# Kernel tuning notes

Measured on AMD Instinct MI355X. Metric: run time of the kernel, lower is better.

The kernel has to match this reference:

```python
import jax, jax.numpy as jnp
import numpy as np
import math

D = 1024
H = 16
EPS = 1e-5

def _layernorm(x, gamma, beta):
    mu = jnp.mean(x, axis=-1, keepdims=True)
    var = jnp.var(x, axis=-1, keepdims=True)
    return (x - mu) * jax.lax.rsqrt(var + EPS) * gamma + beta

def setup_inputs() -> dict:
    key = jax.random.key(0)
    ks = jax.random.split(key, 6)
    B, T = 2, 2048
    x = jax.random.normal(ks[0], (B, T, D), dtype=jnp.float32)
    s = 1.0 / math.sqrt(D)
    Wq = jax.random.normal(ks[1], (D, D), dtype=jnp.float32) * s
    Wk = jax.random.normal(ks[2], (D, D), dtype=jnp.float32) * s
    Wv = jax.random.normal(ks[3], (D, D), dtype=jnp.float32) * s
    gamma = jnp.ones((D,), dtype=jnp.float32)
    beta = jnp.zeros((D,), dtype=jnp.float32)
    return {"x": x, "Wq": Wq, "Wk": Wk, "Wv": Wv, "gamma": gamma, "beta": beta}

def reference(x, Wq, Wk, Wv, gamma, beta):
    B, T, Dm = x.shape
    hd = Dm // H
    xn = _layernorm(x, gamma, beta)
    # torch Linear (no bias): y = x @ W.T
    q = (xn @ Wq.T).reshape(B, T, H, hd)
    k = (xn @ Wk.T).reshape(B, T, H, hd)
    v = (xn @ Wv.T).reshape(B, T, H, hd)
    scale = 1.0 / math.sqrt(hd)
    att = jnp.einsum('bnhd,bmhd->bnmh', q, k) * scale  # B,T,T,H
    w = jax.nn.softmax(att, axis=2)  # softmax over key dim m
    y = jnp.einsum('bnmh,bmhd->bnhd', w, v).reshape(B, T, Dm)
    return x + y
```

## Files before the change

kernel.cpp:

```cpp
#include <hip/hip_runtime.h>
#include <hip/hip_bf16.h>
#include <stdint.h>

#define D_MODEL 1024
#define T_SEQ   2048
#define NB      2
#define NH      16
#define HD      64
#define MTOK    4096

typedef __bf16  bf16x8 __attribute__((ext_vector_type(8)));
typedef float   f32x4  __attribute__((ext_vector_type(4)));
typedef float   f32x16 __attribute__((ext_vector_type(16)));

#define GPTR(p) ((const __attribute__((address_space(1))) void*)(p))
#define LPTR(p) ((__attribute__((address_space(3))) void*)(p))

static __device__ __forceinline__ ushort f2bf(float f) {
    union { float f; uint32_t u; } c{f};
    uint32_t u = c.u;
    return (ushort)((u + 0x7fff + ((u >> 16) & 1)) >> 16);
}

static __device__ __forceinline__ unsigned cvt_pk_bf16(float lo, float hi) {
    unsigned r;
    asm("v_cvt_pk_bf16_f32 %0, %1, %2" : "=v"(r) : "v"(lo), "v"(hi));
    return r;
}

#if defined(__has_builtin)
#if __has_builtin(__builtin_amdgcn_exp2f)
#define FEXP2(x) __builtin_amdgcn_exp2f(x)
#endif
#endif
#ifndef FEXP2
static __device__ __forceinline__ float fexp2_asm(float x) {
    float r;
    asm("v_exp_f32 %0, %1" : "=v"(r) : "v"(x));
    return r;
}
#define FEXP2(x) fexp2_asm(x)
#endif

__global__ __launch_bounds__(256) void prep_kernel(const float* __restrict__ x,
                                                   const float* __restrict__ gamma,
                                                   const float* __restrict__ beta,
                                                   ushort* __restrict__ xn,
                                                   const float* __restrict__ a0,
                                                   const float* __restrict__ a1,
                                                   const float* __restrict__ a2,
                                                   ushort* __restrict__ o0,
                                                   ushort* __restrict__ o1,
                                                   ushort* __restrict__ o2) {
    int blk = blockIdx.x;
    int tid = threadIdx.x;
    if (blk >= MTOK) {
        int z = (blk - MTOK) >> 10;
        int cb = (blk - MTOK) & 1023;
        const float* a = (z == 0) ? a0 : (z == 1) ? a1 : a2;
        ushort* o = (z == 0) ? o0 : (z == 1) ? o1 : o2;
        int i = cb * 256 + tid;
        float4 v = ((const float4*)a)[i];
        ushort4 r;
        r.x = f2bf(v.x); r.y = f2bf(v.y); r.z = f2bf(v.z); r.w = f2bf(v.w);
        ((ushort4*)o)[i] = r;
        return;
    }
    int row = blk;
    const float4* xr = (const float4*)(x + (size_t)row * D_MODEL);
    float4 v = xr[tid];
    float s  = v.x + v.y + v.z + v.w;
    float ss = v.x * v.x + v.y * v.y + v.z * v.z + v.w * v.w;
    #pragma unroll
    for (int m = 1; m < 64; m <<= 1) {
        s  += __shfl_xor(s, m);
        ss += __shfl_xor(ss, m);
    }
    __shared__ float red[8];
    int w = tid >> 6, lane = tid & 63;
    if (lane == 0) { red[w] = s; red[4 + w] = ss; }
    __syncthreads();
    s  = red[0] + red[1] + red[2] + red[3];
    ss = red[4] + red[5] + red[6] + red[7];
    float mu   = s * (1.0f / D_MODEL);
    float var  = ss * (1.0f / D_MODEL) - mu * mu;
    float rstd = rsqrtf(var + 1e-5f);
    float4 g = ((const float4*)gamma)[tid];
    float4 b = ((const float4*)beta)[tid];
    ushort4 o;
    o.x = f2bf((v.x - mu) * rstd * g.x + b.x);
    o.y = f2bf((v.y - mu) * rstd * g.y + b.y);
    o.z = f2bf((v.z - mu) * rstd * g.z + b.z);
    o.w = f2bf((v.w - mu) * rstd * g.w + b.w);
    ((ushort4*)(xn + (size_t)row * D_MODEL))[tid] = o;
}

__global__ __launch_bounds__(256) void gemm_qkv(const ushort* __restrict__ A,
                                                const ushort* __restrict__ w0,
                                                const ushort* __restrict__ w1,
                                                const ushort* __restrict__ w2,
                                                ushort* __restrict__ c0,
                                                ushort* __restrict__ c1,
                                                ushort* __restrict__ c2,
                                                int M, int N, int K) {
    const ushort* Bw = (blockIdx.z == 0) ? w0 : (blockIdx.z == 1) ? w1 : w2;
    ushort* C = (blockIdx.z == 0) ? c0 : (blockIdx.z == 1) ? c1 : c2;

    __shared__ __align__(16) ushort lA[2][128 * 64];
    __shared__ __align__(16) ushort lB[2][128 * 64];
    int tid = threadIdx.x;
    int w = tid >> 6, lane = tid & 63;
    int wr = w >> 1, wc = w & 1;
    int l15 = lane & 15, l4 = lane >> 4;
    int row0 = blockIdx.x * 128, col0 = blockIdx.y * 128;

    f32x4 zero = {0.f, 0.f, 0.f, 0.f};
    f32x4 acc[4][4];
    #pragma unroll
    for (int i = 0; i < 4; ++i)
        #pragma unroll
        for (int j = 0; j < 4; ++j) acc[i][j] = zero;

    int sr  = tid >> 3;
    int scc = (((tid & 7) ^ (sr & 7)) << 3);
    int rch[2];
    rch[0] = ((l4)     ^ (l15 & 7)) << 4;
    rch[1] = ((4 + l4) ^ (l15 & 7)) << 4;

    auto STAGE = [&](int buf, int kt) {
        int k0 = kt * 64;
        #pragma unroll
        for (int i = 0; i < 4; ++i) {
            int r = i * 32 + sr;
            const ushort* ga = A + (size_t)(row0 + r) * K + k0 + scc;
            __builtin_amdgcn_global_load_lds(GPTR(ga), LPTR((char*)lA[buf] + i * 4096 + tid * 16), 16, 0, 0);
            const ushort* gb = Bw + (size_t)(col0 + r) * K + k0 + scc;
            __builtin_amdgcn_global_load_lds(GPTR(gb), LPTR((char*)lB[buf] + i * 4096 + tid * 16), 16, 0, 0);
        }
    };

    STAGE(0, 0);
    __syncthreads();

    int buf = 0;
    const int NK = K / 64;
    for (int kt = 0; kt < NK; ++kt) {
        if (kt + 1 < NK) STAGE(buf ^ 1, kt + 1);
        const char* la  = (const char*)lA[buf];
        const char* lb_ = (const char*)lB[buf];
        __builtin_amdgcn_s_setprio(1);
        #pragma unroll
        for (int ks = 0; ks < 2; ++ks) {
            bf16x8 af[4], bfr[4];
            #pragma unroll
            for (int i = 0; i < 4; ++i) {
                int ra = wr * 64 + i * 16 + l15;
                int rb = wc * 64 + i * 16 + l15;
                af[i]  = *(const bf16x8*)(la  + ra * 128 + rch[ks]);
                bfr[i] = *(const bf16x8*)(lb_ + rb * 128 + rch[ks]);
            }
            #pragma unroll
            for (int i = 0; i < 4; ++i)
                #pragma unroll
                for (int j = 0; j < 4; ++j)
                    acc[i][j] = __builtin_amdgcn_mfma_f32_16x16x32_bf16(af[i], bfr[j], acc[i][j], 0, 0, 0);
        }
        __builtin_amdgcn_s_setprio(0);
        __syncthreads();
        buf ^= 1;
    }

    if (blockIdx.z == 2) {
        #pragma unroll
        for (int i = 0; i < 4; ++i) {
            int rbase = row0 + wr * 64 + i * 16 + l4 * 4;
            #pragma unroll
            for (int j = 0; j < 4; ++j) {
                int col = col0 + wc * 64 + j * 16 + l15;
                ushort4 o4;
                o4.x = f2bf(acc[i][j][0]);
                o4.y = f2bf(acc[i][j][1]);
                o4.z = f2bf(acc[i][j][2]);
                o4.w = f2bf(acc[i][j][3]);
                *(ushort4*)&C[(size_t)col * M + rbase] = o4;
            }
        }
    } else {
        float sc = (blockIdx.z == 0) ? 0.18033688011112042f : 1.0f;
        #pragma unroll
        for (int i = 0; i < 4; ++i) {
            int rbase = row0 + wr * 64 + i * 16 + l4 * 4;
            #pragma unroll
            for (int j = 0; j < 4; ++j) {
                int col = col0 + wc * 64 + j * 16 + l15;
                #pragma unroll
                for (int r = 0; r < 4; ++r)
                    C[(size_t)(rbase + r) * N + col] = f2bf(acc[i][j][r] * sc);
            }
        }
    }
}

__global__ __launch_bounds__(512, 2) void attn_kernel(const ushort* __restrict__ Q,
                                                      const ushort* __restrict__ Km,
                                                      const ushort* __restrict__ Vt,
                                                      const float* __restrict__ x,
                                                      float* __restrict__ out) {
    int bid = blockIdx.x;
    int sw  = (bid & 7) * 32 + (bid >> 3);
    int qt = sw & 7, h = (sw >> 3) & 15, b = sw >> 7;

    int tid = threadIdx.x, w = tid >> 6, lane = tid & 63;
    int l31 = lane & 31, hh = lane >> 5, x7 = lane & 7;
    size_t head_off = (size_t)b * T_SEQ * D_MODEL + (size_t)h * HD;
    const ushort* Qh  = Q  + head_off;
    const ushort* Kh  = Km + head_off;
    const ushort* Vth = Vt + (size_t)h * HD * MTOK + (size_t)b * T_SEQ;

    __shared__ __align__(16) ushort lK[4][64 * 64];
    __shared__ __align__(16) ushort lV[4][64 * 64];

    int qrow = qt * 256 + w * 32 + l31;
    bf16x8 qf[4];
    #pragma unroll
    for (int c = 0; c < 4; ++c)
        qf[c] = *(const bf16x8*)&Qh[(size_t)qrow * D_MODEL + hh * 8 + c * 16];

    int r0  = tid >> 3;
    int cg0 = (tid & 7) ^ (r0 & 7);
    const ushort* ksrc = Kh  + (size_t)r0 * D_MODEL + cg0 * 8;
    const ushort* vsrc = Vth + (size_t)r0 * MTOK + cg0 * 8;

    int chv[4];
    #pragma unroll
    for (int c = 0; c < 4; ++c) chv[c] = ((hh + 2 * c) ^ x7) << 4;

    f32x16 oa[2], ob[2], zvec;
    float la = 0.f, lb = 0.f;
    #pragma unroll
    for (int i = 0; i < 16; ++i) {
        oa[0][i] = 0.f; oa[1][i] = 0.f; ob[0][i] = 0.f; ob[1][i] = 0.f;
        zvec[i] = 0.f;
    }

    auto STAGE = [&](int t) {
        size_t kb = (size_t)t * 64;
        __builtin_amdgcn_global_load_lds(GPTR(ksrc + kb * D_MODEL), LPTR((char*)lK[t & 3] + tid * 16), 16, 0, 0);
        __builtin_amdgcn_global_load_lds(GPTR(vsrc + kb), LPTR((char*)lV[t & 3] + tid * 16), 16, 0, 0);
    };

    auto QK = [&](int t, f32x16& sa, f32x16& sb) {
        const char* lKc = (const char*)lK[t & 3];
        __builtin_amdgcn_s_setprio(1);
        {
            bf16x8 ka  = *(const bf16x8*)(lKc + l31 * 128 + chv[0]);
            bf16x8 kb2 = *(const bf16x8*)(lKc + (32 + l31) * 128 + chv[0]);
            sa = __builtin_amdgcn_mfma_f32_32x32x16_bf16(ka,  qf[0], zvec, 0, 0, 0);
            sb = __builtin_amdgcn_mfma_f32_32x32x16_bf16(kb2, qf[0], zvec, 0, 0, 0);
        }
        #pragma unroll
        for (int c = 1; c < 4; ++c) {
            bf16x8 ka  = *(const bf16x8*)(lKc + l31 * 128 + chv[c]);
            bf16x8 kb2 = *(const bf16x8*)(lKc + (32 + l31) * 128 + chv[c]);
            sa = __builtin_amdgcn_mfma_f32_32x32x16_bf16(ka,  qf[c], sa, 0, 0, 0);
            sb = __builtin_amdgcn_mfma_f32_32x32x16_bf16(kb2, qf[c], sb, 0, 0, 0);
        }
        __builtin_amdgcn_s_setprio(0);
    };

    auto SMPV = [&](int t, const f32x16& sa, const f32x16& sb) {
        const char* lVc = (const char*)lV[t & 3];
        bf16x8 vfr[4][2];
        #pragma unroll
        for (int ks = 0; ks < 4; ++ks)
            #pragma unroll
            for (int dblk = 0; dblk < 2; ++dblk)
                vfr[ks][dblk] = *(const bf16x8*)(lVc + (dblk * 32 + l31) * 128 + chv[ks]);

        bf16x8 pfr[4];
        #pragma unroll
        for (int kbb = 0; kbb < 2; ++kbb) {
            float pr[16];
            #pragma unroll
            for (int r = 0; r < 16; ++r) pr[r] = FEXP2(kbb ? sb[r] : sa[r]);
            float s0 = (pr[0] + pr[1]) + (pr[2] + pr[3]);
            float s1 = (pr[4] + pr[5]) + (pr[6] + pr[7]);
            float s2 = (pr[8] + pr[9]) + (pr[10] + pr[11]);
            float s3 = (pr[12] + pr[13]) + (pr[14] + pr[15]);
            if (kbb == 0) la += (s0 + s1) + (s2 + s3);
            else          lb += (s0 + s1) + (s2 + s3);
            #pragma unroll
            for (int sl = 0; sl < 2; ++sl) {
                unsigned pA = cvt_pk_bf16(pr[sl * 8 + 0], pr[sl * 8 + 1]);
                unsigned pB = cvt_pk_bf16(pr[sl * 8 + 2], pr[sl * 8 + 3]);
                unsigned pC = cvt_pk_bf16(pr[sl * 8 + 4], pr[sl * 8 + 5]);
                unsigned pD = cvt_pk_bf16(pr[sl * 8 + 6], pr[sl * 8 + 7]);
                asm("v_permlane32_swap_b32 %0, %1" : "+v"(pA), "+v"(pC));
                asm("v_permlane32_swap_b32 %0, %1" : "+v"(pB), "+v"(pD));
                union { unsigned u[4]; bf16x8 v; } pf;
                pf.u[0] = pA; pf.u[1] = pB; pf.u[2] = pC; pf.u[3] = pD;
                pfr[kbb * 2 + sl] = pf.v;
            }
        }
        __builtin_amdgcn_s_setprio(1);
        #pragma unroll
        for (int ks = 0; ks < 4; ++ks) {
            #pragma unroll
            for (int dblk = 0; dblk < 2; ++dblk) {
                if (ks & 1)
                    ob[dblk] = __builtin_amdgcn_mfma_f32_32x32x16_bf16(vfr[ks][dblk], pfr[ks], ob[dblk], 0, 0, 0);
                else
                    oa[dblk] = __builtin_amdgcn_mfma_f32_32x32x16_bf16(vfr[ks][dblk], pfr[ks], oa[dblk], 0, 0, 0);
            }
        }
        __builtin_amdgcn_s_setprio(0);
    };

    STAGE(0);
    STAGE(1);
    __syncthreads();

    const int NT = T_SEQ / 64;
    for (int s = 0; s < NT / 2; ++s) {
        int t0 = 2 * s;
        if (s < NT / 2 - 1) { STAGE(t0 + 2); STAGE(t0 + 3); }
        f32x16 sa0, sb0, sa1, sb1;
        QK(t0, sa0, sb0);
        QK(t0 + 1, sa1, sb1);
        SMPV(t0, sa0, sb0);
        SMPV(t0 + 1, sa1, sb1);
        __syncthreads();
    }

    float Lt = la + lb;
    float Lfull = Lt + __shfl_xor(Lt, 32);
    float inv = 1.0f / Lfull;
    const float* xrow = x   + (size_t)(b * T_SEQ + qrow) * D_MODEL + h * HD + 4 * hh;
    float*       orow = out + (size_t)(b * T_SEQ + qrow) * D_MODEL + h * HD + 4 * hh;
    #pragma unroll
    for (int dblk = 0; dblk < 2; ++dblk) {
        #pragma unroll
        for (int g = 0; g < 4; ++g) {
            int coff = dblk * 32 + 8 * g;
            float4 xv = *(const float4*)(xrow + coff);
            float4 ov;
            ov.x = xv.x + (oa[dblk][4 * g + 0] + ob[dblk][4 * g + 0]) * inv;
            ov.y = xv.y + (oa[dblk][4 * g + 1] + ob[dblk][4 * g + 1]) * inv;
            ov.z = xv.z + (oa[dblk][4 * g + 2] + ob[dblk][4 * g + 2]) * inv;
            ov.w = xv.w + (oa[dblk][4 * g + 3] + ob[dblk][4 * g + 3]) * inv;
            *(float4*)(orow + coff) = ov;
        }
    }
}

extern "C" void kernel_launch(void* const* d_in, const int* in_sizes, int n_in,
                              void* d_out, int out_size, void* d_ws, size_t ws_size,
                              hipStream_t stream) {
    const float* x     = (const float*)d_in[0];
    const float* Wq    = (const float*)d_in[1];
    const float* Wk    = (const float*)d_in[2];
    const float* Wv    = (const float*)d_in[3];
    const float* gamma = (const float*)d_in[4];
    const float* beta  = (const float*)d_in[5];
    float* out = (float*)d_out;

    char* ws = (char*)d_ws;
    ushort* xn  = (ushort*)(ws);
    ushort* wqb = (ushort*)(ws + (8  << 20));
    ushort* wkb = (ushort*)(ws + (10 << 20));
    ushort* wvb = (ushort*)(ws + (12 << 20));
    ushort* Qb  = (ushort*)(ws + (14 << 20));
    ushort* Kb  = (ushort*)(ws + (22 << 20));
    ushort* Vtb = (ushort*)(ws + (30 << 20));

    int M = NB * T_SEQ;

    prep_kernel<<<dim3(MTOK + 3072), 256, 0, stream>>>(x, gamma, beta, xn,
                                                       Wq, Wk, Wv, wqb, wkb, wvb);
    gemm_qkv<<<dim3(M / 128, D_MODEL / 128, 3), 256, 0, stream>>>(
        xn, wqb, wkb, wvb, Qb, Kb, Vtb, M, D_MODEL, D_MODEL);
    attn_kernel<<<dim3(256), 512, 0, stream>>>(Qb, Kb, Vtb, x, out);
}
```

Measured before the change: 96.15 us.

## Give each attention wave two query groups sharing K/V fragments, halve block size

The attention kernel now runs 256 threads per block, and each wave handles 64 query rows as two 32-row groups. K and V fragments are read from LDS once and reused for both groups, which halves LDS reads per unit of MFMA work. Each thread stages two rows per tile to keep the loads covered. Explicit vmcnt(0) waits are added before the barriers in both the GEMM and attention kernels so the async LDS loads are known to be complete. The cost is more accumulator and fragment registers per wave and fewer waves per CU, so there is less latency hiding.

```diff
diff --git a/kernel.cpp b/kernel.cpp
--- a/kernel.cpp
+++ b/kernel.cpp
@@ -15,6 +15,7 @@
 
 #define GPTR(p) ((const __attribute__((address_space(1))) void*)(p))
 #define LPTR(p) ((__attribute__((address_space(3))) void*)(p))
+#define VMCNT0() asm volatile("s_waitcnt vmcnt(0)" ::: "memory")
 
 static __device__ __forceinline__ ushort f2bf(float f) {
     union { float f; uint32_t u; } c{f};
@@ -140,6 +141,7 @@
     };
 
     STAGE(0, 0);
+    VMCNT0();
     __syncthreads();
 
     int buf = 0;
@@ -166,6 +168,7 @@
                     acc[i][j] = __builtin_amdgcn_mfma_f32_16x16x32_bf16(af[i], bfr[j], acc[i][j], 0, 0, 0);
         }
         __builtin_amdgcn_s_setprio(0);
+        VMCNT0();
         __syncthreads();
         buf ^= 1;
     }
@@ -201,7 +204,7 @@
     }
 }
 
-__global__ __launch_bounds__(512, 2) void attn_kernel(const ushort* __restrict__ Q,
+__global__ __launch_bounds__(256, 1) void attn_kernel(const ushort* __restrict__ Q,
                                                       const ushort* __restrict__ Km,
                                                       const ushort* __restrict__ Vt,
                                                       const float* __restrict__ x,
@@ -220,135 +223,149 @@
     __shared__ __align__(16) ushort lK[4][64 * 64];
     __shared__ __align__(16) ushort lV[4][64 * 64];
 
-    int qrow = qt * 256 + w * 32 + l31;
-    bf16x8 qf[4];
-    #pragma unroll
-    for (int c = 0; c < 4; ++c)
-        qf[c] = *(const bf16x8*)&Qh[(size_t)qrow * D_MODEL + hh * 8 + c * 16];
+    bf16x8 qf[2][4];
+    #pragma unroll
+    for (int qg = 0; qg < 2; ++qg) {
+        int qrow = qt * 256 + w * 64 + qg * 32 + l31;
+        #pragma unroll
+        for (int c = 0; c < 4; ++c)
+            qf[qg][c] = *(const bf16x8*)&Qh[(size_t)qrow * D_MODEL + hh * 8 + c * 16];
+    }
 
     int r0  = tid >> 3;
     int cg0 = (tid & 7) ^ (r0 & 7);
-    const ushort* ksrc = Kh  + (size_t)r0 * D_MODEL + cg0 * 8;
-    const ushort* vsrc = Vth + (size_t)r0 * MTOK + cg0 * 8;
+    const ushort* ksrcA = Kh  + (size_t)r0 * D_MODEL + cg0 * 8;
+    const ushort* ksrcB = ksrcA + (size_t)32 * D_MODEL;
+    const ushort* vsrcA = Vth + (size_t)r0 * MTOK + cg0 * 8;
+    const ushort* vsrcB = vsrcA + (size_t)32 * MTOK;
 
     int chv[4];
     #pragma unroll
     for (int c = 0; c < 4; ++c) chv[c] = ((hh + 2 * c) ^ x7) << 4;
 
-    f32x16 oa[2], ob[2], zvec;
-    float la = 0.f, lb = 0.f;
+    f32x16 o[2][2], zvec;
+    float la[2] = {0.f, 0.f};
     #pragma unroll
     for (int i = 0; i < 16; ++i) {
-        oa[0][i] = 0.f; oa[1][i] = 0.f; ob[0][i] = 0.f; ob[1][i] = 0.f;
+        o[0][0][i] = 0.f; o[0][1][i] = 0.f; o[1][0][i] = 0.f; o[1][1][i] = 0.f;
         zvec[i] = 0.f;
     }
 
     auto STAGE = [&](int t) {
         size_t kb = (size_t)t * 64;
-        __builtin_amdgcn_global_load_lds(GPTR(ksrc + kb * D_MODEL), LPTR((char*)lK[t & 3] + tid * 16), 16, 0, 0);
-        __builtin_amdgcn_global_load_lds(GPTR(vsrc + kb), LPTR((char*)lV[t & 3] + tid * 16), 16, 0, 0);
+        char* dk = (char*)lK[t & 3];
+        char* dv = (char*)lV[t & 3];
+        __builtin_amdgcn_global_load_lds(GPTR(ksrcA + kb * D_MODEL), LPTR(dk + tid * 16), 16, 0, 0);
+        __builtin_amdgcn_global_load_lds(GPTR(ksrcB + kb * D_MODEL), LPTR(dk + (tid + 256) * 16), 16, 0, 0);
+        __builtin_amdgcn_global_load_lds(GPTR(vsrcA + kb), LPTR(dv + tid * 16), 16, 0, 0);
+        __builtin_amdgcn_global_load_lds(GPTR(vsrcB + kb), LPTR(dv + (tid + 256) * 16), 16, 0, 0);
     };
 
-    auto QK = [&](int t, f32x16& sa, f32x16& sb) {
+    auto COMPUTE = [&](int t) {
         const char* lKc = (const char*)lK[t & 3];
+        const char* lVc = (const char*)lV[t & 3];
+
+        bf16x8 kfr[2][4];
+        #pragma unroll
+        for (int c = 0; c < 4; ++c) {
+            kfr[0][c] = *(const bf16x8*)(lKc + l31 * 128 + chv[c]);
+            kfr[1][c] = *(const bf16x8*)(lKc + (32 + l31) * 128 + chv[c]);
+        }
+        f32x16 s[2][2];
         __builtin_amdgcn_s_setprio(1);
-        {
-            bf16x8 ka  = *(const bf16x8*)(lKc + l31 * 128 + chv[0]);
-            bf16x8 kb2 = *(const bf16x8*)(lKc + (32 + l31) * 128 + chv[0]);
-            sa = __builtin_amdgcn_mfma_f32_32x32x16_bf16(ka,  qf[0], zvec, 0, 0, 0);
-            sb = __builtin_amdgcn_mfma_f32_32x32x16_bf16(kb2, qf[0], zvec, 0, 0, 0);
-        }
-        #pragma unroll
-        for (int c = 1; c < 4; ++c) {
-            bf16x8 ka  = *(const bf16x8*)(lKc + l31 * 128 + chv[c]);
-            bf16x8 kb2 = *(const bf16x8*)(lKc + (32 + l31) * 128 + chv[c]);
-            sa = __builtin_amdgcn_mfma_f32_32x32x16_bf16(ka,  qf[c], sa, 0, 0, 0);
-            sb = __builtin_amdgcn_mfma_f32_32x32x16_bf16(kb2, qf[c], sb, 0, 0, 0);
-        }
+        #pragma unroll
+        for (int qg = 0; qg < 2; ++qg) {
+            s[qg][0] = __builtin_amdgcn_mfma_f32_32x32x16_bf16(kfr[0][0], qf[qg][0], zvec, 0, 0, 0);
+            s[qg][1] = __builtin_amdgcn_mfma_f32_32x32x16_bf16(kfr[1][0], qf[qg][0], zvec, 0, 0, 0);
+            #pragma unroll
+            for (int c = 1; c < 4; ++c) {
+                s[qg][0] = __builtin_amdgcn_mfma_f32_32x32x16_bf16(kfr[0][c], qf[qg][c], s[qg][0], 0, 0, 0);
+                s[qg][1] = __builtin_amdgcn_mfma_f32_32x32x16_bf16(kfr[1][c], qf[qg][c], s[qg][1], 0, 0, 0);
+            }
+        }
+        __builtin_amdgcn_s_setprio(0);
+
+        bf16x8 pfr[2][4];
+        #pragma unroll
+        for (int qg = 0; qg < 2; ++qg) {
+            #pragma unroll
+            for (int half = 0; half < 2; ++half) {
+                float pr[16];
+                #pragma unroll
+                for (int r = 0; r < 16; ++r) pr[r] = FEXP2(s[qg][half][r]);
+                float s0 = (pr[0] + pr[1]) + (pr[2] + pr[3]);
+                float s1 = (pr[4] + pr[5]) + (pr[6] + pr[7]);
+                float s2 = (pr[8] + pr[9]) + (pr[10] + pr[11]);
+                float s3 = (pr[12] + pr[13]) + (pr[14] + pr[15]);
+                la[qg] += (s0 + s1) + (s2 + s3);
+                #pragma unroll
+                for (int sl = 0; sl < 2; ++sl) {
+                    unsigned pA = cvt_pk_bf16(pr[sl * 8 + 0], pr[sl * 8 + 1]);
+                    unsigned pB = cvt_pk_bf16(pr[sl * 8 + 2], pr[sl * 8 + 3]);
+                    unsigned pC = cvt_pk_bf16(pr[sl * 8 + 4], pr[sl * 8 + 5]);
+                    unsigned pD = cvt_pk_bf16(pr[sl * 8 + 6], pr[sl * 8 + 7]);
+                    asm("v_permlane32_swap_b32 %0, %1" : "+v"(pA), "+v"(pC));
+                    asm("v_permlane32_swap_b32 %0, %1" : "+v"(pB), "+v"(pD));
+                    union { unsigned u[4]; bf16x8 v; } pf;
+                    pf.u[0] = pA; pf.u[1] = pB; pf.u[2] = pC; pf.u[3] = pD;
+                    pfr[qg][half * 2 + sl] = pf.v;
+                }
+            }
+        }
+
+        bf16x8 vfr[4][2];
+        #pragma unroll
+        for (int ks = 0; ks < 4; ++ks)
+            #pragma unroll
+            for (int dblk = 0; dblk < 2; ++dblk)
+                vfr[ks][dblk] = *(const bf16x8*)(lVc + (dblk * 32 + l31) * 128 + chv[ks]);
+        __builtin_amdgcn_s_setprio(1);
+        #pragma unroll
+        for (int ks = 0; ks < 4; ++ks)
+            #pragma unroll
+            for (int qg = 0; qg < 2; ++qg)
+                #pragma unroll
+                for (int dblk = 0; dblk < 2; ++dblk)
+                    o[qg][dblk] = __builtin_amdgcn_mfma_f32_32x32x16_bf16(vfr[ks][dblk], pfr[qg][ks], o[qg][dblk], 0, 0, 0);
         __builtin_amdgcn_s_setprio(0);
     };
 
-    auto SMPV = [&](int t, const f32x16& sa, const f32x16& sb) {
-        const char* lVc = (const char*)lV[t & 3];
-        bf16x8 vfr[4][2];
-        #pragma unroll
-        for (int ks = 0; ks < 4; ++ks)
-            #pragma unroll
-            for (int dblk = 0; dblk < 2; ++dblk)
-                vfr[ks][dblk] = *(const bf16x8*)(lVc + (dblk * 32 + l31) * 128 + chv[ks]);
-
-        bf16x8 pfr[4];
-        #pragma unroll
-        for (int kbb = 0; kbb < 2; ++kbb) {
-            float pr[16];
-            #pragma unroll
-            for (int r = 0; r < 16; ++r) pr[r] = FEXP2(kbb ? sb[r] : sa[r]);
-            float s0 = (pr[0] + pr[1]) + (pr[2] + pr[3]);
-            float s1 = (pr[4] + pr[5]) + (pr[6] + pr[7]);
-            float s2 = (pr[8] + pr[9]) + (pr[10] + pr[11]);
-            float s3 = (pr[12] + pr[13]) + (pr[14] + pr[15]);
-            if (kbb == 0) la += (s0 + s1) + (s2 + s3);
-            else          lb += (s0 + s1) + (s2 + s3);
-            #pragma unroll
-            for (int sl = 0; sl < 2; ++sl) {
-                unsigned pA = cvt_pk_bf16(pr[sl * 8 + 0], pr[sl * 8 + 1]);
-                unsigned pB = cvt_pk_bf16(pr[sl * 8 + 2], pr[sl * 8 + 3]);
-                unsigned pC = cvt_pk_bf16(pr[sl * 8 + 4], pr[sl * 8 + 5]);
-                unsigned pD = cvt_pk_bf16(pr[sl * 8 + 6], pr[sl * 8 + 7]);
-                asm("v_permlane32_swap_b32 %0, %1" : "+v"(pA), "+v"(pC));
-                asm("v_permlane32_swap_b32 %0, %1" : "+v"(pB), "+v"(pD));
-                union { unsigned u[4]; bf16x8 v; } pf;
-                pf.u[0] = pA; pf.u[1] = pB; pf.u[2] = pC; pf.u[3] = pD;
-                pfr[kbb * 2 + sl] = pf.v;
-            }
-        }
-        __builtin_amdgcn_s_setprio(1);
-        #pragma unroll
-        for (int ks = 0; ks < 4; ++ks) {
-            #pragma unroll
-            for (int dblk = 0; dblk < 2; ++dblk) {
-                if (ks & 1)
-                    ob[dblk] = __builtin_amdgcn_mfma_f32_32x32x16_bf16(vfr[ks][dblk], pfr[ks], ob[dblk], 0, 0, 0);
-                else
-                    oa[dblk] = __builtin_amdgcn_mfma_f32_32x32x16_bf16(vfr[ks][dblk], pfr[ks], oa[dblk], 0, 0, 0);
-            }
-        }
-        __builtin_amdgcn_s_setprio(0);
-    };
-
     STAGE(0);
     STAGE(1);
+    VMCNT0();
     __syncthreads();
 
     const int NT = T_SEQ / 64;
-    for (int s = 0; s < NT / 2; ++s) {
-        int t0 = 2 * s;
-        if (s < NT / 2 - 1) { STAGE(t0 + 2); STAGE(t0 + 3); }
-        f32x16 sa0, sb0, sa1, sb1;
-        QK(t0, sa0, sb0);
-        QK(t0 + 1, sa1, sb1);
-        SMPV(t0, sa0, sb0);
-        SMPV(t0 + 1, sa1, sb1);
+    for (int sp = 0; sp < NT / 2; ++sp) {
+        int t0 = 2 * sp;
+        if (sp < NT / 2 - 1) { STAGE(t0 + 2); STAGE(t0 + 3); }
+        COMPUTE(t0);
+        COMPUTE(t0 + 1);
+        VMCNT0();
         __syncthreads();
     }
 
-    float Lt = la + lb;
-    float Lfull = Lt + __shfl_xor(Lt, 32);
-    float inv = 1.0f / Lfull;
-    const float* xrow = x   + (size_t)(b * T_SEQ + qrow) * D_MODEL + h * HD + 4 * hh;
-    float*       orow = out + (size_t)(b * T_SEQ + qrow) * D_MODEL + h * HD + 4 * hh;
-    #pragma unroll
-    for (int dblk = 0; dblk < 2; ++dblk) {
-        #pragma unroll
-        for (int g = 0; g < 4; ++g) {
-            int coff = dblk * 32 + 8 * g;
-            float4 xv = *(const float4*)(xrow + coff);
-            float4 ov;
-            ov.x = xv.x + (oa[dblk][4 * g + 0] + ob[dblk][4 * g + 0]) * inv;
-            ov.y = xv.y + (oa[dblk][4 * g + 1] + ob[dblk][4 * g + 1]) * inv;
-            ov.z = xv.z + (oa[dblk][4 * g + 2] + ob[dblk][4 * g + 2]) * inv;
-            ov.w = xv.w + (oa[dblk][4 * g + 3] + ob[dblk][4 * g + 3]) * inv;
-            *(float4*)(orow + coff) = ov;
+    #pragma unroll
+    for (int qg = 0; qg < 2; ++qg) {
+        float Lt = la[qg];
+        float Lfull = Lt + __shfl_xor(Lt, 32);
+        float inv = 1.0f / Lfull;
+        int qrow = qt * 256 + w * 64 + qg * 32 + l31;
+        const float* xrow = x   + (size_t)(b * T_SEQ + qrow) * D_MODEL + h * HD + 4 * hh;
+        float*       orow = out + (size_t)(b * T_SEQ + qrow) * D_MODEL + h * HD + 4 * hh;
+        #pragma unroll
+        for (int dblk = 0; dblk < 2; ++dblk) {
+            #pragma unroll
+            for (int g = 0; g < 4; ++g) {
+                int coff = dblk * 32 + 8 * g;
+                float4 xv = *(const float4*)(xrow + coff);
+                float4 ov;
+                ov.x = xv.x + o[qg][dblk][4 * g + 0] * inv;
+                ov.y = xv.y + o[qg][dblk][4 * g + 1] * inv;
+                ov.z = xv.z + o[qg][dblk][4 * g + 2] * inv;
+                ov.w = xv.w + o[qg][dblk][4 * g + 3] * inv;
+                *(float4*)(orow + coff) = ov;
+            }
         }
     }
 }
@@ -379,5 +396,5 @@
                                                        Wq, Wk, Wv, wqb, wkb, wvb);
     gemm_qkv<<<dim3(M / 128, D_MODEL / 128, 3), 256, 0, stream>>>(
         xn, wqb, wkb, wvb, Qb, Kb, Vtb, M, D_MODEL, D_MODEL);
-    attn_kernel<<<dim3(256), 512, 0, stream>>>(Qb, Kb, Vtb, x, out);
-}
+    attn_kernel<<<dim3(256), 256, 0, stream>>>(Qb, Kb, Vtb, x, out);
+}
```

Result: slower. 108.8 us (+13.1%).
